# Kernel tuning notes

Measured on AMD Instinct MI355X. Metric: run time of the kernel, lower is better.

The kernel has to match this reference:

```python
import jax, jax.numpy as jnp
import numpy as np

N, E, D, L, G = 50000, 1600000, 128, 3, 64


def setup_inputs() -> dict:
    key = jax.random.key(0)
    ks = jax.random.split(key, 10)
    s = 1.0 / np.sqrt(D).astype(np.float32)
    X = jax.random.normal(ks[0], (N, D), jnp.float32)
    edge_index = jax.random.randint(ks[1], (2, E), 0, N, dtype=jnp.int32)
    edge_types = jax.random.randint(ks[2], (E,), 0, 2, dtype=jnp.int32)
    batch_ids = jnp.sort(jax.random.randint(ks[3], (N,), 0, G, dtype=jnp.int32))
    Wd = jax.random.uniform(ks[4], (L, D, D), jnp.float32, -s, s)
    bd = jax.random.uniform(ks[5], (L, D), jnp.float32, -s, s)
    Wc = jax.random.uniform(ks[6], (L, D, D), jnp.float32, -s, s)
    bc = jax.random.uniform(ks[7], (L, D), jnp.float32, -s, s)
    Ws = jax.random.uniform(ks[8], (L, D, D), jnp.float32, -s, s)
    bs = jax.random.uniform(ks[9], (L, D), jnp.float32, -s, s)
    return dict(X=X, Wd=Wd, bd=bd, Wc=Wc, bc=bc, Ws=Ws, bs=bs,
                edge_index=edge_index, edge_types=edge_types, batch_ids=batch_ids)


def reference(X, Wd, bd, Wc, bc, Ws, bs, edge_index, edge_types, batch_ids):
    src, dst = edge_index[0], edge_index[1]
    is_data = (edge_types == 0)[:, None]  # [E,1] edge-type selector
    for l in range(L):
        # Linear commutes with gather: compute node-level GEMMs once,
        # then per-edge gather + type select (same math as per-edge Linear).
        Xd = X @ Wd[l] + bd[l]            # [N,D] data-edge messages
        Xc = X @ Wc[l] + bc[l]            # [N,D] control-edge messages
        msg = jnp.where(is_data, Xd[src], Xc[src])      # [E,D]
        agg = jax.ops.segment_sum(msg, dst, num_segments=N)  # scatter-add
        X = jax.nn.relu(agg + X @ Ws[l] + bs[l])
    # global mean pool per graph
    sums = jax.ops.segment_sum(X, batch_ids, num_segments=G)
    cnts = jax.ops.segment_sum(jnp.ones((N,), X.dtype), batch_ids, num_segments=G)
    return sums / jnp.maximum(cnts, 1.0)[:, None]
```

## Files before the change

kernel.cpp:

```cpp
#include <hip/hip_runtime.h>
#include <hip/hip_fp16.h>

#define N_NODES 50000
#define N_EDGES 1600000
#define DIM     128
#define NLAYERS 3
#define NGRAPHS 64

#define NBUCK   196
#define CSR_BLKS 256
#define EPB     (N_EDGES / CSR_BLKS)
#define EITER   ((EPB + 255) / 256)

typedef _Float16 half8 __attribute__((ext_vector_type(8)));
typedef float    f32x4 __attribute__((ext_vector_type(4)));
typedef float    f32x2 __attribute__((ext_vector_type(2)));

#define LDK 136

__device__ __forceinline__ unsigned char f32_to_fp8(float v) {
    int q = __builtin_amdgcn_cvt_pk_fp8_f32(v, v, 0, false);
    return (unsigned char)(q & 0xFF);
}

__global__ __launch_bounds__(256) void setup_kernel(
        const float* __restrict__ X, __half* __restrict__ Xh,
        unsigned char* __restrict__ X8,
        const float* __restrict__ Wd, const float* __restrict__ Wc,
        const float* __restrict__ Ws, __half* __restrict__ WT,
        float* __restrict__ sums, int* __restrict__ gcnt) {
    int i = blockIdx.x * 256 + threadIdx.x;
    if (i < N_NODES * DIM / 4) {
        float4 v = *(const float4*)(X + (size_t)i * 4);
        union { __half2 h2[2]; uint2 u; } pk;
        pk.h2[0] = __floats2half2_rn(v.x, v.y);
        pk.h2[1] = __floats2half2_rn(v.z, v.w);
        *(uint2*)(Xh + (size_t)i * 4) = pk.u;
        int q0 = __builtin_amdgcn_cvt_pk_fp8_f32(v.x, v.y, 0, false);
        int q1 = __builtin_amdgcn_cvt_pk_fp8_f32(v.z, v.w, q0, true);
        *(unsigned int*)(X8 + (size_t)i * 4) = (unsigned int)q1;
    }
    if (i < 9 * DIM * DIM) {
        int k  = i & 127;
        int n  = (i >> 7) & 127;
        int lw = i >> 14;
        int l  = lw / 3, w = lw - 3 * l;
        const float* W = ((w == 0) ? Wd : (w == 1) ? Wc : Ws)
                         + (size_t)l * DIM * DIM;
        WT[i] = __float2half(W[k * DIM + n]);
    }
    if (i < NGRAPHS * DIM) sums[i] = 0.f;
    if (i < NGRAPHS) gcnt[i] = 0;
}

__global__ __launch_bounds__(256) void csr1_kernel(const int* __restrict__ dst,
                                                   int* __restrict__ cntmat) {
    __shared__ int hc[NBUCK];
    int tid = threadIdx.x;
    for (int i = tid; i < NBUCK; i += 256) hc[i] = 0;
    __syncthreads();
    int base = blockIdx.x * EPB;
#pragma unroll
    for (int i = 0; i < EITER; ++i) {
        int idx = i * 256 + tid;
        if (idx < EPB) atomicAdd(&hc[dst[base + idx] >> 8], 1);
    }
    __syncthreads();
    for (int i = tid; i < NBUCK; i += 256)
        cntmat[i * CSR_BLKS + blockIdx.x] = hc[i];
}

__global__ __launch_bounds__(256) void scanA_kernel(const int* __restrict__ cntmat,
                                                    int* __restrict__ exc,
                                                    int* __restrict__ btot) {
    __shared__ int sh[256];
    int tid = threadIdx.x, b = blockIdx.x;
    int v = cntmat[b * CSR_BLKS + tid];
    sh[tid] = v;
    __syncthreads();
    for (int o = 1; o < 256; o <<= 1) {
        int t = (tid >= o) ? sh[tid - o] : 0;
        __syncthreads();
        sh[tid] += t;
        __syncthreads();
    }
    exc[b * CSR_BLKS + tid] = sh[tid] - v;
    if (tid == 255) btot[b] = sh[255];
}

__global__ __launch_bounds__(256) void csr2_kernel(const int* __restrict__ src,
                                                   const int* __restrict__ dst,
                                                   const int* __restrict__ et,
                                                   const int* __restrict__ exc,
                                                   const int* __restrict__ btot,
                                                   int* __restrict__ bstart,
                                                   int* __restrict__ esv) {
    __shared__ int sh[256];
    __shared__ int bst[NBUCK];
    __shared__ int cur[NBUCK];
    int tid = threadIdx.x;
    int v = (tid < NBUCK) ? btot[tid] : 0;
    sh[tid] = v;
    __syncthreads();
    for (int o = 1; o < 256; o <<= 1) {
        int t = (tid >= o) ? sh[tid - o] : 0;
        __syncthreads();
        sh[tid] += t;
        __syncthreads();
    }
    if (tid < NBUCK) bst[tid] = sh[tid] - v;
    if (blockIdx.x == 0) {
        if (tid < NBUCK) bstart[tid] = sh[tid] - v;
        if (tid == NBUCK - 1) bstart[NBUCK] = sh[tid];
    }
    __syncthreads();
    if (tid < NBUCK) cur[tid] = exc[tid * CSR_BLKS + blockIdx.x] + bst[tid];
    __syncthreads();
    int base = blockIdx.x * EPB;
#pragma unroll
    for (int i = 0; i < EITER; ++i) {
        int idx = i * 256 + tid;
        if (idx < EPB) {
            int e = base + idx;
            int d = dst[e];
            int pos = atomicAdd(&cur[d >> 8], 1);
            esv[pos] = (src[e] + et[e] * N_NODES) | ((d & 255) << 17);
        }
    }
}

__global__ __launch_bounds__(256) void csr3_kernel(const int* __restrict__ esv,
                                                   const int* __restrict__ bstart,
                                                   int* __restrict__ col,
                                                   int* __restrict__ row_start,
                                                   int* __restrict__ deg,
                                                   int* __restrict__ degd) {
    __shared__ int cnt[256];
    __shared__ int cntd[256];
    __shared__ int sh[256];
    __shared__ int cur[256];
    int tid = threadIdx.x, b = blockIdx.x;
    int bs = bstart[b], be = bstart[b + 1];
    cnt[tid] = 0;
    cntd[tid] = 0;
    __syncthreads();
    for (int e = bs + tid; e < be; e += 256) {
        int pk = esv[e];
        int nd = (pk >> 17) & 255;
        atomicAdd(&cnt[nd], 1);
        if ((pk & 0x1FFFF) < N_NODES) atomicAdd(&cntd[nd], 1);
    }
    __syncthreads();
    int v = cnt[tid];
    sh[tid] = v;
    __syncthreads();
    for (int o = 1; o < 256; o <<= 1) {
        int t = (tid >= o) ? sh[tid - o] : 0;
        __syncthreads();
        sh[tid] += t;
        __syncthreads();
    }
    int off  = sh[tid] - v;
    int node = (b << 8) + tid;
    if (node < N_NODES) {
        row_start[node] = bs + off;
        deg[node]       = v;
        degd[node]      = cntd[tid];
    }
    cur[tid] = bs + off;
    __syncthreads();
    for (int e = bs + tid; e < be; e += 256) {
        int pk  = esv[e];
        int nd  = (pk >> 17) & 255;
        int pos = atomicAdd(&cur[nd], 1);
        col[pos] = pk & 0x1FFFF;
    }
}

__global__ __launch_bounds__(256) void agg_kernel(
        const int* __restrict__ row_start, const int* __restrict__ deg_arr,
        const int* __restrict__ col,
        const unsigned char* __restrict__ X8,
        __half* __restrict__ Sd, __half* __restrict__ Sc) {
    int wave = (blockIdx.x * 256 + threadIdx.x) >> 6;
    int lane = threadIdx.x & 63;
    int grp  = lane >> 4;
    int l16  = lane & 15;
    int node = wave * 4 + grp;
    if (node >= N_NODES) return;

    int rs  = row_start[node];
    int deg = deg_arr[node];
    const size_t off = (size_t)l16 * 8;

    float aT[8], aD[8];
#pragma unroll
    for (int j = 0; j < 8; ++j) { aT[j] = 0.f; aD[j] = 0.f; }

    if (deg > 0) {
        int dgm1 = deg - 1;
        int nb   = (deg + 7) >> 3;
        int p[8];
#pragma unroll
        for (int i = 0; i < 8; ++i)
            p[i] = col[rs + (i < deg ? i : dgm1)];
        for (int b = 0; b < nb; ++b) {
            int e0 = b * 8;
            uint2 v[8];
            int  c[8];
#pragma unroll
            for (int i = 0; i < 8; ++i) {
                int pi  = p[i];
                int isC = pi >= N_NODES;
                int row = pi - (isC ? N_NODES : 0);
                c[i] = isC;
                v[i] = *(const uint2*)(X8 + (size_t)row * DIM + off);
            }
            int pn[8];
            if (b + 1 < nb) {
                int e1 = e0 + 8;
#pragma unroll
                for (int i = 0; i < 8; ++i) {
                    int idx = e1 + i;
                    pn[i] = col[rs + (idx < deg ? idx : dgm1)];
                }
            }
#pragma unroll
            for (int i = 0; i < 8; ++i) {
                if (e0 + i >= deg) { v[i].x = 0u; v[i].y = 0u; }
            }
#pragma unroll
            for (int i = 0; i < 8; ++i) {
                unsigned int dx = c[i] ? 0u : v[i].x;
                unsigned int dy = c[i] ? 0u : v[i].y;
                f32x2 t0 = __builtin_amdgcn_cvt_pk_f32_fp8(v[i].x, false);
                f32x2 t1 = __builtin_amdgcn_cvt_pk_f32_fp8(v[i].x, true);
                f32x2 t2 = __builtin_amdgcn_cvt_pk_f32_fp8(v[i].y, false);
                f32x2 t3 = __builtin_amdgcn_cvt_pk_f32_fp8(v[i].y, true);
                aT[0] += t0[0]; aT[1] += t0[1];
                aT[2] += t1[0]; aT[3] += t1[1];
                aT[4] += t2[0]; aT[5] += t2[1];
                aT[6] += t3[0]; aT[7] += t3[1];
                f32x2 d0 = __builtin_amdgcn_cvt_pk_f32_fp8(dx, false);
                f32x2 d1 = __builtin_amdgcn_cvt_pk_f32_fp8(dx, true);
                f32x2 d2 = __builtin_amdgcn_cvt_pk_f32_fp8(dy, false);
                f32x2 d3 = __builtin_amdgcn_cvt_pk_f32_fp8(dy, true);
                aD[0] += d0[0]; aD[1] += d0[1];
                aD[2] += d1[0]; aD[3] += d1[1];
                aD[4] += d2[0]; aD[5] += d2[1];
                aD[6] += d3[0]; aD[7] += d3[1];
            }
            if (b + 1 < nb) {
#pragma unroll
                for (int i = 0; i < 8; ++i) p[i] = pn[i];
            }
        }
    }

    union { __half2 h2[4]; uint4 u; } pd, pc;
#pragma unroll
    for (int j = 0; j < 4; ++j) {
        pd.h2[j] = __floats2half2_rn(aD[2 * j], aD[2 * j + 1]);
        pc.h2[j] = __floats2half2_rn(aT[2 * j] - aD[2 * j],
                                     aT[2 * j + 1] - aD[2 * j + 1]);
    }
    *(uint4*)(Sd + (size_t)node * DIM + off) = pd.u;
    *(uint4*)(Sc + (size_t)node * DIM + off) = pc.u;
}

__global__ __launch_bounds__(256) void gemm_fused_kernel(
        const __half* __restrict__ Sd, const __half* __restrict__ Sc,
        const __half* __restrict__ Xh,
        const __half* __restrict__ WTl,
        const float* __restrict__ bd, const float* __restrict__ bc,
        const float* __restrict__ bs,
        const int* __restrict__ degd, const int* __restrict__ deg,
        __half* __restrict__ Xh_out, unsigned char* __restrict__ X8_out,
        int write8) {
    __shared__ _Float16 As[64 * LDK];
    __shared__ _Float16 Bs[128 * LDK];

    const int tid = threadIdx.x;
    const int m0  = blockIdx.x * 64;

    const int wv = tid >> 6;
    const int l  = tid & 63;
    const int lm = l & 15;
    const int q  = l >> 4;

    f32x4 acc[4][2];
#pragma unroll
    for (int mt = 0; mt < 4; ++mt) {
        acc[mt][0] = (f32x4){0.f, 0.f, 0.f, 0.f};
        acc[mt][1] = (f32x4){0.f, 0.f, 0.f, 0.f};
    }

    for (int w = 0; w < 3; ++w) {
        if (w) __syncthreads();
        const __half* Asrc = (w == 0) ? Sd : (w == 1) ? Sc : Xh;
#pragma unroll
        for (int i = 0; i < 4; ++i) {
            int c    = i * 256 + tid;
            int row  = c >> 4;
            int colh = (c & 15) * 8;
            uint4 v  = make_uint4(0u, 0u, 0u, 0u);
            int gr   = m0 + row;
            if (gr < N_NODES) v = *(const uint4*)(Asrc + (size_t)gr * DIM + colh);
            *(uint4*)(As + row * LDK + colh) = v;
        }
        {
            const __half* Wt = WTl + (size_t)w * DIM * DIM;
#pragma unroll
            for (int i = 0; i < 8; ++i) {
                int c    = i * 256 + tid;
                int row  = c >> 4;
                int colh = (c & 15) * 8;
                uint4 v = *(const uint4*)(Wt + (size_t)row * DIM + colh);
                *(uint4*)(Bs + row * LDK + colh) = v;
            }
        }
        __syncthreads();

#pragma unroll
        for (int ks = 0; ks < 4; ++ks) {
            int coff = ks * 32 + q * 8;
            half8 am[4];
#pragma unroll
            for (int mt = 0; mt < 4; ++mt)
                am[mt] = *(const half8*)(As + (mt * 16 + lm) * LDK + coff);
            half8 bb0 = *(const half8*)(Bs + (wv * 32 + lm) * LDK + coff);
            half8 bb1 = *(const half8*)(Bs + (wv * 32 + 16 + lm) * LDK + coff);
#pragma unroll
            for (int mt = 0; mt < 4; ++mt) {
                acc[mt][0] = __builtin_amdgcn_mfma_f32_16x16x32_f16(am[mt], bb0, acc[mt][0], 0, 0, 0);
                acc[mt][1] = __builtin_amdgcn_mfma_f32_16x16x32_f16(am[mt], bb1, acc[mt][1], 0, 0, 0);
            }
        }
    }

    const int colg0 = wv * 32 + lm;
    const int colg1 = wv * 32 + 16 + lm;
    float bd0 = bd[colg0], bd1 = bd[colg1];
    float bc0 = bc[colg0], bc1 = bc[colg1];
    float bs0 = bs[colg0], bs1 = bs[colg1];
#pragma unroll
    for (int mt = 0; mt < 4; ++mt) {
#pragma unroll
        for (int r = 0; r < 4; ++r) {
            int row = m0 + mt * 16 + q * 4 + r;
            if (row < N_NODES) {
                float dd = (float)degd[row];
                float dc = (float)(deg[row] - degd[row]);
                float v0 = fmaxf(acc[mt][0][r] + dd * bd0 + dc * bc0 + bs0, 0.f);
                float v1 = fmaxf(acc[mt][1][r] + dd * bd1 + dc * bc1 + bs1, 0.f);
                Xh_out[(size_t)row * DIM + colg0] = __float2half(v0);
                Xh_out[(size_t)row * DIM + colg1] = __float2half(v1);
                if (write8) {
                    X8_out[(size_t)row * DIM + colg0] = f32_to_fp8(v0);
                    X8_out[(size_t)row * DIM + colg1] = f32_to_fp8(v1);
                }
            }
        }
    }
}

__global__ __launch_bounds__(256) void pool_kernel(const __half* __restrict__ X,
                                                   const int* __restrict__ bid,
                                                   float* __restrict__ sums,
                                                   int* __restrict__ gcnt) {
    __shared__ float acc[8][DIM];
    __shared__ int scnt[8];
    __shared__ int sgmin;
    int tid = threadIdx.x;
    for (int i = tid; i < 8 * DIM; i += 256) ((float*)acc)[i] = 0.f;
    if (tid < 8) scnt[tid] = 0;
    int n0 = blockIdx.x * 64;
    if (tid == 0) sgmin = bid[n0];
    __syncthreads();
    int gmin = sgmin;

    int s    = tid >> 5;
    int lane = tid & 31;
    int r0   = n0 + s * 8;

    int g[8];
    union { uint2 u; __half2 h2[2]; } v[8];
#pragma unroll
    for (int i = 0; i < 8; ++i) {
        int r = r0 + i;
        g[i] = (r < N_NODES) ? bid[r] : -1;
    }
#pragma unroll
    for (int i = 0; i < 8; ++i) {
        int r = r0 + i;
        if (r < N_NODES)
            v[i].u = *(const uint2*)(X + (size_t)r * DIM + lane * 4);
        else { v[i].u.x = 0u; v[i].u.y = 0u; }
    }

    float4 a = make_float4(0.f, 0.f, 0.f, 0.f);
    int cur = -1, run = 0;
#pragma unroll
    for (int i = 0; i < 8; ++i) {
        if (g[i] != cur) {
            if (cur >= 0) {
                int slot = cur - gmin;
                if (slot < 8) {
                    atomicAdd(&acc[slot][lane * 4 + 0], a.x);
                    atomicAdd(&acc[slot][lane * 4 + 1], a.y);
                    atomicAdd(&acc[slot][lane * 4 + 2], a.z);
                    atomicAdd(&acc[slot][lane * 4 + 3], a.w);
                    if (lane == 0) atomicAdd(&scnt[slot], run);
                } else {
                    atomicAdd(&sums[cur * DIM + lane * 4 + 0], a.x);
                    atomicAdd(&sums[cur * DIM + lane * 4 + 1], a.y);
                    atomicAdd(&sums[cur * DIM + lane * 4 + 2], a.z);
                    atomicAdd(&sums[cur * DIM + lane * 4 + 3], a.w);
                    if (lane == 0) atomicAdd(&gcnt[cur], run);
                }
            }
            cur = g[i];
            a = make_float4(0.f, 0.f, 0.f, 0.f);
            run = 0;
        }
        if (g[i] >= 0) {
            float2 f0 = __half22float2(v[i].h2[0]);
            float2 f1 = __half22float2(v[i].h2[1]);
            a.x += f0.x; a.y += f0.y; a.z += f1.x; a.w += f1.y;
            run++;
        }
    }
    if (cur >= 0) {
        int slot = cur - gmin;
        if (slot < 8) {
            atomicAdd(&acc[slot][lane * 4 + 0], a.x);
            atomicAdd(&acc[slot][lane * 4 + 1], a.y);
            atomicAdd(&acc[slot][lane * 4 + 2], a.z);
            atomicAdd(&acc[slot][lane * 4 + 3], a.w);
            if (lane == 0) atomicAdd(&scnt[slot], run);
        } else {
            atomicAdd(&sums[cur * DIM + lane * 4 + 0], a.x);
            atomicAdd(&sums[cur * DIM + lane * 4 + 1], a.y);
            atomicAdd(&sums[cur * DIM + lane * 4 + 2], a.z);
            atomicAdd(&sums[cur * DIM + lane * 4 + 3], a.w);
            if (lane == 0) atomicAdd(&gcnt[cur], run);
        }
    }
    __syncthreads();

    for (int slot = 0; slot < 8; ++slot) {
        if (scnt[slot] > 0) {
            int gg = gmin + slot;
            for (int i = tid; i < DIM; i += 256)
                atomicAdd(&sums[gg * DIM + i], acc[slot][i]);
            if (tid == 0) atomicAdd(&gcnt[gg], scnt[slot]);
        }
    }
}

__global__ __launch_bounds__(256) void div_kernel(const float* __restrict__ sums,
                                                  const int* __restrict__ gcnt,
                                                  float* __restrict__ out) {
    int i = blockIdx.x * 256 + threadIdx.x;
    if (i < NGRAPHS * DIM) {
        int g = i >> 7;
        out[i] = sums[i] / fmaxf((float)gcnt[g], 1.f);
    }
}

extern "C" void kernel_launch(void* const* d_in, const int* in_sizes, int n_in,
                              void* d_out, int out_size, void* d_ws, size_t ws_size,
                              hipStream_t stream) {
    const float* Xin = (const float*)d_in[0];
    const float* Wd  = (const float*)d_in[1];
    const float* bd  = (const float*)d_in[2];
    const float* Wc  = (const float*)d_in[3];
    const float* bc  = (const float*)d_in[4];
    const float* Ws  = (const float*)d_in[5];
    const float* bs  = (const float*)d_in[6];
    const int* edge_index = (const int*)d_in[7];
    const int* edge_types = (const int*)d_in[8];
    const int* batch_ids  = (const int*)d_in[9];

    const int* src = edge_index;
    const int* dst = edge_index + N_EDGES;

    const size_t NBH = (size_t)N_NODES * DIM * sizeof(__half);
    const size_t NB8 = (size_t)N_NODES * DIM;
    char* w = (char*)d_ws;
    auto take = [&](size_t bytes) {
        char* p = w;
        w += (bytes + 255) & ~(size_t)255;
        return p;
    };
    __half* Xh0  = (__half*)take(NBH);
    __half* Xh1  = (__half*)take(NBH);
    unsigned char* X8a = (unsigned char*)take(NB8);
    unsigned char* X8b = (unsigned char*)take(NB8);
    __half* SdB  = (__half*)take(NBH);
    __half* ScB  = (__half*)take(NBH);
    __half* WT   = (__half*)take((size_t)9 * DIM * DIM * sizeof(__half));
    int* col     = (int*)take((size_t)N_EDGES * 4);
    int* esv     = (int*)take((size_t)N_EDGES * 4);
    int* cntmat  = (int*)take((size_t)NBUCK * CSR_BLKS * 4);
    int* exc     = (int*)take((size_t)NBUCK * CSR_BLKS * 4);
    int* btot    = (int*)take((size_t)NBUCK * 4);
    int* bstart  = (int*)take((size_t)(NBUCK + 1) * 4);
    int* rowst   = (int*)take((size_t)N_NODES * 4);
    int* deg     = (int*)take((size_t)N_NODES * 4);
    int* degd    = (int*)take((size_t)N_NODES * 4);
    float* sums  = (float*)take((size_t)NGRAPHS * DIM * 4);
    int* gcnt    = (int*)take(NGRAPHS * 4);

    setup_kernel<<<(N_NODES * DIM / 4 + 255) / 256, 256, 0, stream>>>(
        Xin, Xh0, X8a, Wd, Wc, Ws, WT, sums, gcnt);

    csr1_kernel<<<CSR_BLKS, 256, 0, stream>>>(dst, cntmat);
    scanA_kernel<<<NBUCK, 256, 0, stream>>>(cntmat, exc, btot);
    csr2_kernel<<<CSR_BLKS, 256, 0, stream>>>(src, dst, edge_types, exc,
                                              btot, bstart, esv);
    csr3_kernel<<<NBUCK, 256, 0, stream>>>(esv, bstart, col, rowst, deg, degd);

    const int GEMM_MBLK = (N_NODES + 63) / 64;
    const int AGG_BLKS  = (N_NODES + 15) / 16;

    const __half*      Xhc = Xh0;
    const unsigned char* X8c = X8a;
    __half*            XhN[3] = {Xh1, Xh0, Xh1};
    unsigned char*     X8N[3] = {X8b, X8a, X8b};
    for (int l = 0; l < NLAYERS; ++l) {
        agg_kernel<<<AGG_BLKS, 256, 0, stream>>>(rowst, deg, col, X8c, SdB, ScB);
        gemm_fused_kernel<<<GEMM_MBLK, 256, 0, stream>>>(
            SdB, ScB, Xhc, WT + (size_t)l * 3 * DIM * DIM,
            bd + (size_t)l * DIM, bc + (size_t)l * DIM, bs + (size_t)l * DIM,
            degd, deg, XhN[l], X8N[l], (l < NLAYERS - 1) ? 1 : 0);
        Xhc = XhN[l];
        X8c = X8N[l];
    }

    const int POOL_BLKS = (N_NODES + 63) / 64;
    pool_kernel<<<POOL_BLKS, 256, 0, stream>>>(Xhc, batch_ids, sums, gcnt);
    div_kernel<<<(NGRAPHS * DIM + 255) / 256, 256, 0, stream>>>(sums, gcnt,
                                                                (float*)d_out);
}
```

Before: 335.1 us.

## Partition CSR by edge type and vectorize transposed GEMM epilogue stores

The CSR build now places each node's data edges before its control edges and stores plain source indices. This lets the aggregation kernel sum two separate ranges into two accumulators, dropping the per-edge select and the second FP8 conversion pass. The GEMM swaps its MFMA operands so each lane holds four consecutive columns of one row. The epilogue can then use vector bias loads, packed half2 stores and packed FP8 conversion instead of scalar byte and half stores. Splitting each node's edges into two ranges adds loop overhead and tail padding per node.

```diff
diff --git a/kernel.cpp b/kernel.cpp
--- a/kernel.cpp
+++ b/kernel.cpp
@@ -138,7 +138,8 @@
     __shared__ int cnt[256];
     __shared__ int cntd[256];
     __shared__ int sh[256];
-    __shared__ int cur[256];
+    __shared__ int curD[256];
+    __shared__ int curC[256];
     int tid = threadIdx.x, b = blockIdx.x;
     int bs = bstart[b], be = bstart[b + 1];
     cnt[tid] = 0;
@@ -167,19 +168,68 @@
         deg[node]       = v;
         degd[node]      = cntd[tid];
     }
-    cur[tid] = bs + off;
+    curD[tid] = bs + off;
+    curC[tid] = bs + off + cntd[tid];
     __syncthreads();
     for (int e = bs + tid; e < be; e += 256) {
         int pk  = esv[e];
         int nd  = (pk >> 17) & 255;
-        int pos = atomicAdd(&cur[nd], 1);
-        col[pos] = pk & 0x1FFFF;
+        int sv  = pk & 0x1FFFF;
+        int isC = sv >= N_NODES;
+        int pos = atomicAdd(isC ? &curC[nd] : &curD[nd], 1);
+        col[pos] = sv - (isC ? N_NODES : 0);
+    }
+}
+
+__device__ __forceinline__ void agg_range(
+        const int* __restrict__ col, const unsigned char* __restrict__ X8,
+        unsigned off, int base, int cnt, float* a) {
+    if (cnt <= 0) return;
+    int last = cnt - 1;
+    int nb = (cnt + 7) >> 3;
+    int p[8];
+#pragma unroll
+    for (int i = 0; i < 8; ++i)
+        p[i] = col[base + (i < cnt ? i : last)];
+    for (int b = 0; b < nb; ++b) {
+        int e0 = b * 8;
+        uint2 v[8];
+#pragma unroll
+        for (int i = 0; i < 8; ++i)
+            v[i] = *(const uint2*)(X8 + (((unsigned)p[i] << 7) | off));
+        int pn[8];
+        if (b + 1 < nb) {
+            int e1 = e0 + 8;
+#pragma unroll
+            for (int i = 0; i < 8; ++i) {
+                int idx = e1 + i;
+                pn[i] = col[base + (idx < cnt ? idx : last)];
+            }
+        }
+#pragma unroll
+        for (int i = 0; i < 8; ++i)
+            if (e0 + i >= cnt) { v[i].x = 0u; v[i].y = 0u; }
+#pragma unroll
+        for (int i = 0; i < 8; ++i) {
+            f32x2 f0 = __builtin_amdgcn_cvt_pk_f32_fp8(v[i].x, false);
+            f32x2 f1 = __builtin_amdgcn_cvt_pk_f32_fp8(v[i].x, true);
+            f32x2 f2 = __builtin_amdgcn_cvt_pk_f32_fp8(v[i].y, false);
+            f32x2 f3 = __builtin_amdgcn_cvt_pk_f32_fp8(v[i].y, true);
+            a[0] += f0[0]; a[1] += f0[1];
+            a[2] += f1[0]; a[3] += f1[1];
+            a[4] += f2[0]; a[5] += f2[1];
+            a[6] += f3[0]; a[7] += f3[1];
+        }
+        if (b + 1 < nb) {
+#pragma unroll
+            for (int i = 0; i < 8; ++i) p[i] = pn[i];
+        }
     }
 }
 
 __global__ __launch_bounds__(256) void agg_kernel(
         const int* __restrict__ row_start, const int* __restrict__ deg_arr,
-        const int* __restrict__ col,
+        const int* __restrict__ degd_arr, const int* __restrict__ col,
         const unsigned char* __restrict__ X8,
         __half* __restrict__ Sd, __half* __restrict__ Sc) {
     int wave = (blockIdx.x * 256 + threadIdx.x) >> 6;
@@ -189,80 +239,23 @@
     int node = wave * 4 + grp;
     if (node >= N_NODES) return;
 
-    int rs  = row_start[node];
-    int deg = deg_arr[node];
-    const size_t off = (size_t)l16 * 8;
-
-    float aT[8], aD[8];
-#pragma unroll
-    for (int j = 0; j < 8; ++j) { aT[j] = 0.f; aD[j] = 0.f; }
-
-    if (deg > 0) {
-        int dgm1 = deg - 1;
-        int nb   = (deg + 7) >> 3;
-        int p[8];
-#pragma unroll
-        for (int i = 0; i < 8; ++i)
-            p[i] = col[rs + (i < deg ? i : dgm1)];
-        for (int b = 0; b < nb; ++b) {
-            int e0 = b * 8;
-            uint2 v[8];
-            int  c[8];
-#pragma unroll
-            for (int i = 0; i < 8; ++i) {
-                int pi  = p[i];
-                int isC = pi >= N_NODES;
-                int row = pi - (isC ? N_NODES : 0);
-                c[i] = isC;
-                v[i] = *(const uint2*)(X8 + (size_t)row * DIM + off);
-            }
-            int pn[8];
-            if (b + 1 < nb) {
-                int e1 = e0 + 8;
-#pragma unroll
-                for (int i = 0; i < 8; ++i) {
-                    int idx = e1 + i;
-                    pn[i] = col[rs + (idx < deg ? idx : dgm1)];
-                }
-            }
-#pragma unroll
-            for (int i = 0; i < 8; ++i) {
-                if (e0 + i >= deg) { v[i].x = 0u; v[i].y = 0u; }
-            }
-#pragma unroll
-            for (int i = 0; i < 8; ++i) {
-                unsigned int dx = c[i] ? 0u : v[i].x;
-                unsigned int dy = c[i] ? 0u : v[i].y;
-                f32x2 t0 = __builtin_amdgcn_cvt_pk_f32_fp8(v[i].x, false);
-                f32x2 t1 = __builtin_amdgcn_cvt_pk_f32_fp8(v[i].x, true);
-                f32x2 t2 = __builtin_amdgcn_cvt_pk_f32_fp8(v[i].y, false);
-                f32x2 t3 = __builtin_amdgcn_cvt_pk_f32_fp8(v[i].y, true);
-                aT[0] += t0[0]; aT[1] += t0[1];
-                aT[2] += t1[0]; aT[3] += t1[1];
-                aT[4] += t2[0]; aT[5] += t2[1];
-                aT[6] += t3[0]; aT[7] += t3[1];
-                f32x2 d0 = __builtin_amdgcn_cvt_pk_f32_fp8(dx, false);
-                f32x2 d1 = __builtin_amdgcn_cvt_pk_f32_fp8(dx, true);
-                f32x2 d2 = __builtin_amdgcn_cvt_pk_f32_fp8(dy, false);
-                f32x2 d3 = __builtin_amdgcn_cvt_pk_f32_fp8(dy, true);
-                aD[0] += d0[0]; aD[1] += d0[1];
-                aD[2] += d1[0]; aD[3] += d1[1];
-                aD[4] += d2[0]; aD[5] += d2[1];
-                aD[6] += d3[0]; aD[7] += d3[1];
-            }
-            if (b + 1 < nb) {
-#pragma unroll
-                for (int i = 0; i < 8; ++i) p[i] = pn[i];
-            }
-        }
-    }
+    int rs = row_start[node];
+    int dg = deg_arr[node];
+    int dd = degd_arr[node];
+    const unsigned off = (unsigned)l16 * 8;
+
+    float aD[8], aC[8];
+#pragma unroll
+    for (int j = 0; j < 8; ++j) { aD[j] = 0.f; aC[j] = 0.f; }
+
+    agg_range(col, X8, off, rs, dd, aD);
+    agg_range(col, X8, off, rs + dd, dg - dd, aC);
 
     union { __half2 h2[4]; uint4 u; } pd, pc;
 #pragma unroll
     for (int j = 0; j < 4; ++j) {
         pd.h2[j] = __floats2half2_rn(aD[2 * j], aD[2 * j + 1]);
-        pc.h2[j] = __floats2half2_rn(aT[2 * j] - aD[2 * j],
-                                     aT[2 * j + 1] - aD[2 * j + 1]);
+        pc.h2[j] = __floats2half2_rn(aC[2 * j], aC[2 * j + 1]);
     }
     *(uint4*)(Sd + (size_t)node * DIM + off) = pd.u;
     *(uint4*)(Sc + (size_t)node * DIM + off) = pc.u;
@@ -332,33 +325,43 @@
             half8 bb1 = *(const half8*)(Bs + (wv * 32 + 16 + lm) * LDK + coff);
 #pragma unroll
             for (int mt = 0; mt < 4; ++mt) {
-                acc[mt][0] = __builtin_amdgcn_mfma_f32_16x16x32_f16(am[mt], bb0, acc[mt][0], 0, 0, 0);
-                acc[mt][1] = __builtin_amdgcn_mfma_f32_16x16x32_f16(am[mt], bb1, acc[mt][1], 0, 0, 0);
+                acc[mt][0] = __builtin_amdgcn_mfma_f32_16x16x32_f16(bb0, am[mt], acc[mt][0], 0, 0, 0);
+                acc[mt][1] = __builtin_amdgcn_mfma_f32_16x16x32_f16(bb1, am[mt], acc[mt][1], 0, 0, 0);
             }
         }
     }
 
-    const int colg0 = wv * 32 + lm;
-    const int colg1 = wv * 32 + 16 + lm;
-    float bd0 = bd[colg0], bd1 = bd[colg1];
-    float bc0 = bc[colg0], bc1 = bc[colg1];
-    float bs0 = bs[colg0], bs1 = bs[colg1];
+    const int fb0 = wv * 32 + q * 4;
+    const int fb1 = fb0 + 16;
+    f32x4 bdv0 = *(const f32x4*)(bd + fb0), bdv1 = *(const f32x4*)(bd + fb1);
+    f32x4 bcv0 = *(const f32x4*)(bc + fb0), bcv1 = *(const f32x4*)(bc + fb1);
+    f32x4 bsv0 = *(const f32x4*)(bs + fb0), bsv1 = *(const f32x4*)(bs + fb1);
 #pragma unroll
     for (int mt = 0; mt < 4; ++mt) {
-#pragma unroll
-        for (int r = 0; r < 4; ++r) {
-            int row = m0 + mt * 16 + q * 4 + r;
-            if (row < N_NODES) {
-                float dd = (float)degd[row];
-                float dc = (float)(deg[row] - degd[row]);
-                float v0 = fmaxf(acc[mt][0][r] + dd * bd0 + dc * bc0 + bs0, 0.f);
-                float v1 = fmaxf(acc[mt][1][r] + dd * bd1 + dc * bc1 + bs1, 0.f);
-                Xh_out[(size_t)row * DIM + colg0] = __float2half(v0);
-                Xh_out[(size_t)row * DIM + colg1] = __float2half(v1);
-                if (write8) {
-                    X8_out[(size_t)row * DIM + colg0] = f32_to_fp8(v0);
-                    X8_out[(size_t)row * DIM + colg1] = f32_to_fp8(v1);
-                }
+        int row = m0 + mt * 16 + lm;
+        if (row < N_NODES) {
+            float dd = (float)degd[row];
+            float dc = (float)(deg[row] - degd[row]);
+            float v0[4], v1[4];
+#pragma unroll
+            for (int r = 0; r < 4; ++r) {
+                v0[r] = fmaxf(acc[mt][0][r] + dd * bdv0[r] + dc * bcv0[r] + bsv0[r], 0.f);
+                v1[r] = fmaxf(acc[mt][1][r] + dd * bdv1[r] + dc * bcv1[r] + bsv1[r], 0.f);
+            }
+            union { __half2 h2[2]; uint2 u; } p0, p1;
+            p0.h2[0] = __floats2half2_rn(v0[0], v0[1]);
+            p0.h2[1] = __floats2half2_rn(v0[2], v0[3]);
+            p1.h2[0] = __floats2half2_rn(v1[0], v1[1]);
+            p1.h2[1] = __floats2half2_rn(v1[2], v1[3]);
+            *(uint2*)(Xh_out + (size_t)row * DIM + fb0) = p0.u;
+            *(uint2*)(Xh_out + (size_t)row * DIM + fb1) = p1.u;
+            if (write8) {
+                int q0 = __builtin_amdgcn_cvt_pk_fp8_f32(v0[0], v0[1], 0, false);
+                q0 = __builtin_amdgcn_cvt_pk_fp8_f32(v0[2], v0[3], q0, true);
+                int q1 = __builtin_amdgcn_cvt_pk_fp8_f32(v1[0], v1[1], 0, false);
+                q1 = __builtin_amdgcn_cvt_pk_fp8_f32(v1[2], v1[3], q1, true);
+                *(unsigned int*)(X8_out + (size_t)row * DIM + fb0) = (unsigned)q0;
+                *(unsigned int*)(X8_out + (size_t)row * DIM + fb1) = (unsigned)q1;
             }
         }
     }
@@ -529,7 +532,8 @@
     __half*            XhN[3] = {Xh1, Xh0, Xh1};
     unsigned char*     X8N[3] = {X8b, X8a, X8b};
     for (int l = 0; l < NLAYERS; ++l) {
-        agg_kernel<<<AGG_BLKS, 256, 0, stream>>>(rowst, deg, col, X8c, SdB, ScB);
+        agg_kernel<<<AGG_BLKS, 256, 0, stream>>>(rowst, deg, degd, col, X8c,
+                                                 SdB, ScB);
         gemm_fused_kernel<<<GEMM_MBLK, 256, 0, stream>>>(
             SdB, ScB, Xhc, WT + (size_t)l * 3 * DIM * DIM,
             bd + (size_t)l * DIM, bc + (size_t)l * DIM, bs + (size_t)l * DIM,
```

Result: faster. 314.3 us (-6.2%).
